# Kernel tuning notes

Measured on AMD Instinct MI355X. Metric: run time of the kernel, lower is better.

The kernel has to match this reference:

```python
import jax, jax.numpy as jnp
import numpy as np

BIT = 64
N_CLASS = 100
NUM_TRAIN = 100000
BATCH = 512
MU = 1.0   # config['mu']
M = 1.0    # config['m']
ETA = 0.5  # config['eta']
VUL = 1.0  # config['vul']
NTA = 1.0  # config['nta']


def setup_inputs() -> dict:
    key = jax.random.key(0)
    k1, k2, k3, k4, k5, k6 = jax.random.split(key, 6)
    u = jax.random.normal(k1, (BATCH, BIT), jnp.float32)
    # y / Y are one-hot label matrices in DFH; build realistic one-hot floats
    labels = jax.random.randint(k2, (BATCH,), 0, N_CLASS)
    y = jax.nn.one_hot(labels, N_CLASS, dtype=jnp.float32)
    ind = jax.random.randint(k3, (BATCH,), 0, NUM_TRAIN)
    U = jax.random.normal(k4, (BIT, NUM_TRAIN), jnp.float32)
    train_labels = jax.random.randint(k5, (NUM_TRAIN,), 0, N_CLASS)
    Y = jax.nn.one_hot(train_labels, N_CLASS, dtype=jnp.float32).T  # [n_class, num_train]
    V = jax.random.normal(k6, (BIT, N_CLASS), jnp.float32)
    return {"u": u, "y": y, "ind": ind, "U": U, "Y": Y, "V": V}


def _center_gradient(V, y, b):
    # 200-step gradient descent on V minimizing intra + vul*inter + nta*quant.
    n_class = V.shape[1]
    TK = V.shape[0] * (2.0 * jnp.eye(n_class, dtype=V.dtype)
                       - jnp.ones((n_class, n_class), V.dtype))
    yt = y.T  # [n_class, batch]

    def inner_loss(Vc):
        intra = jnp.mean((Vc @ yt - b) ** 2)
        inter = jnp.mean((Vc.T @ Vc - TK) ** 2)
        quant = jnp.mean((Vc - jnp.sign(Vc)) ** 2)
        return intra + VUL * inter + NTA * quant

    grad_fn = jax.grad(inner_loss)

    def step(Vc, i):
        # torch code multiplies alpha by 0.1 *before* the update at i==149 and i==179
        alpha = 0.03 * jnp.where(i >= 149, 0.1, 1.0) * jnp.where(i >= 179, 0.1, 1.0)
        return Vc - alpha * grad_fn(Vc), None

    V_new, _ = jax.lax.scan(step, V, jnp.arange(200))
    return V_new


def reference(u, y, ind, U, Y, V):
    # state buffer updates (torch: self.U[:, ind] = u.t().data, etc.)
    U = U.at[:, ind].set(u.T)
    Y = Y.at[:, ind].set(y.T)
    C = jnp.sign(V)
    b = jnp.sign(MU * (C @ y.T) + u.T)                     # [bit, batch]
    V_new = _center_gradient(V, y, b)                      # updated self.V
    s = (y @ Y > 0).astype(u.dtype)                        # [batch, num_train]
    ip = jnp.clip(0.5 * (u @ U), -100.0, 50.0)             # [batch, num_train]
    metric_loss = jnp.mean((1.0 - s) * jnp.log1p(jnp.exp(M + ip))
                           + s * jnp.log1p(jnp.exp(M - ip)))
    quantization_loss = jnp.mean((b - u.T) ** 2)
    loss = metric_loss + ETA * quantization_loss
    return loss, V_new
```

## Files before the change

kernel.cpp:

```cpp
#include <hip/hip_runtime.h>

#define BIT 64
#define NCLASS 100
#define NTRAIN 100000
#define BATCH 512

#define O_OWNER   0
#define O_LAB     200000
#define O_BSUM    233280
#define O_COUNT   239680
#define O_QSUM    239780
#define O_MSUM    239782

typedef __attribute__((ext_vector_type(8))) short short8v;
typedef __attribute__((ext_vector_type(4))) float f32x4;
typedef unsigned short ushortT;

__device__ __forceinline__ float signf(float x) {
    return (x > 0.f) ? 1.f : ((x < 0.f) ? -1.f : 0.f);
}

__device__ __forceinline__ unsigned cvtpk(float lo, float hi) {
    unsigned r;
    asm("v_cvt_pk_bf16_f32 %0, %1, %2" : "=v"(r) : "v"(lo), "v"(hi));
    return r;
}
__device__ __forceinline__ float dpp_x1(float x) {
    union { float f; int i; } v; v.f = x;
    v.i = __builtin_amdgcn_mov_dpp(v.i, 0xB1, 0xF, 0xF, false);
    return v.f;
}
__device__ __forceinline__ float dpp_x2(float x) {
    union { float f; int i; } v; v.f = x;
    v.i = __builtin_amdgcn_mov_dpp(v.i, 0x4E, 0xF, 0xF, false);
    return v.f;
}

__global__ __launch_bounds__(512) void k_pre(
        const float* __restrict__ y, const int* __restrict__ ind,
        const float* __restrict__ u, const float* __restrict__ V,
        int* owner, int* lab, float* Bsum, float* count, double* qsum) {
    __shared__ float srow[BATCH];
    __shared__ int   labl[BATCH];
    __shared__ double wq[8];
    const int r = blockIdx.x;
    const int bb = threadIdx.x;

    const float* yrow = y + bb * NCLASS;
    int best = 0;
    for (int c = 0; c < NCLASS; ++c)
        if (yrow[c] > 0.5f) best = c;
    labl[bb] = best;
    if (r == 0) {
        lab[bb] = best;
        atomicMax(&owner[ind[bb]], bb);
    }

    const float v  = V[r * NCLASS + best];
    const float uu = u[bb * BIT + r];
    const float bv = signf(signf(v) + uu);
    srow[bb] = bv;
    const float d = bv - uu;
    double q = (double)(d * d);
    for (int off = 32; off; off >>= 1) q += __shfl_down(q, off);
    const int wid = bb >> 6, lane = bb & 63;
    if (lane == 0) wq[wid] = q;
    __syncthreads();
    if (bb == 0) {
        double s = 0;
        for (int w = 0; w < 8; ++w) s += wq[w];
        atomicAdd(qsum, s);
    }

    if (bb < NCLASS) {
        float s = 0.f; int n = 0;
        for (int k = 0; k < BATCH; ++k) {
            const bool hit = (labl[k] == bb);
            s += hit ? srow[k] : 0.f;
            n += hit;
        }
        Bsum[r * NCLASS + bb] = s;
        if (r == 0) count[bb] = (float)n;
    }
}

__global__ __launch_bounds__(512, 2) void k_main(
        const float* __restrict__ V, const float* __restrict__ Bsum,
        const float* __restrict__ count, const float* __restrict__ u,
        const float* __restrict__ U, const float* __restrict__ Y,
        const int* __restrict__ lab, const int* __restrict__ owner,
        double* msum, float* __restrict__ out) {
    __shared__ __align__(16) char smem[81920];

    if (blockIdx.x == 0) {
        ushortT* SAb = (ushortT*)smem;
        ushortT* SBb = (ushortT*)(smem + 32768);
        ushortT* SMf = (ushortT*)(smem + 61440);
        float*   rs  = (float*)(smem + 69632);

        const int t = threadIdx.x, l = t & 63, w = t >> 6;
        const int g = l >> 4, c16 = l & 15;
        const int h = w >> 2;
        const int mtile = w & 3;
        const int m = mtile * 16 + c16;
        const bool dg = ((mtile >> 1) == h);
        const short8v ONES = {0x3F80,0x3F80,0x3F80,0x3F80,
                              0x3F80,0x3F80,0x3F80,0x3F80};

        for (int i = t; i < 16384; i += 512) SAb[i] = 0;
        for (int i = t; i < 14336; i += 512) SBb[i] = 0;

        const float ci = 2.0f / 32768.0f;
        const float ce = 4.0f / 10000.0f;
        const float cq = 2.0f / 6400.0f;
        const float ce64 = 64.0f * ce;

        bool live[4], wact[4];
        int sbO[4];
        float vreg[4][4], Kc[4][4], ncib[4][4];
        #pragma unroll
        for (int q = 0; q < 4; ++q) {
            const int nt = 4 * h + q;
            const int n0 = nt * 16 + 4 * g;
            wact[q] = (nt < 7);
            live[q] = wact[q] && (n0 < NCLASS);
            sbO[q] = ((nt * 2 + (mtile >> 1)) * 64 +
                      (16 * (c16 >> 2) + 4 * g + (c16 & 3))) * 8 + 4 * (mtile & 1);
            #pragma unroll
            for (int r = 0; r < 4; ++r) {
                float v = 0.f, bs = 0.f, cn = 0.f;
                if (live[q]) {
                    const int n = n0 + r;
                    v  = V[m * NCLASS + n];
                    bs = Bsum[m * NCLASS + n];
                    cn = count[n];
                }
                vreg[q][r] = v;
                Kc[q][r]   = ci * cn + cq - 128.f * ce;
                ncib[q][r] = -ci * bs;
            }
        }
        const int saO0 = (mtile * 4 + 2 * h) * 512 + l * 8;
        const int saO1 = saO0 + 512;

        uint4 waA, waB;

        auto store_frags = [&](ushortT* SAn, ushortT* SBn) {
            waA.x = cvtpk(vreg[0][0], vreg[0][1]);
            waA.y = cvtpk(vreg[0][2], vreg[0][3]);
            waA.z = cvtpk(vreg[1][0], vreg[1][1]);
            waA.w = cvtpk(vreg[1][2], vreg[1][3]);
            *(uint4*)&SAn[saO0] = waA;
            waB.x = cvtpk(vreg[2][0], vreg[2][1]);
            waB.y = cvtpk(vreg[2][2], vreg[2][3]);
            waB.z = cvtpk(vreg[3][0], vreg[3][1]);
            waB.w = cvtpk(vreg[3][2], vreg[3][3]);
            *(uint4*)&SAn[saO1] = waB;
            #pragma unroll
            for (int q = 0; q < 4; ++q) {
                if (wact[q]) {
                    float a0 = vreg[q][0], a1 = vreg[q][1];
                    float a2 = vreg[q][2], a3 = vreg[q][3];
                    float t0 = dpp_x1(a1), t1 = dpp_x1(a0);
                    float t2 = dpp_x1(a3), t3 = dpp_x1(a2);
                    const bool o1 = (l & 1);
                    float c0 = o1 ? t0 : a0;
                    float c1 = o1 ? a1 : t1;
                    float c2 = o1 ? t2 : a2;
                    float c3 = o1 ? a3 : t3;
                    float u0 = dpp_x2(c2), u1 = dpp_x2(c3);
                    float u2 = dpp_x2(c0), u3 = dpp_x2(c1);
                    const bool o2 = (l & 2);
                    float d0 = o2 ? u0 : c0;
                    float d1 = o2 ? u1 : c1;
                    float d2 = o2 ? c2 : u2;
                    float d3 = o2 ? c3 : u3;
                    uint2 wb;
                    wb.x = cvtpk(d0, d1);
                    wb.y = cvtpk(d2, d3);
                    *(uint2*)&SBn[sbO[q]] = wb;
                }
            }
        };

        __syncthreads();
        store_frags(SAb, SBb);
        __syncthreads();

        int cur = 0;
        for (int step = 0; step < 200; ++step) {
            float alpha = 0.03f;
            if (step >= 149) alpha *= 0.1f;
            if (step >= 179) alpha *= 0.1f;

            const ushortT* SAc = SAb + cur * 8192;
            const ushortT* SBc = SBb + cur * 7168;

            short8v a0[4], a1[4], bx0, bx1;
            #pragma unroll
            for (int ks = 0; ks < 4; ++ks) {
                a0[ks] = *(const short8v*)&SAc[(2 * h) * 2048 + ks * 512 + l * 8];
                a1[ks] = *(const short8v*)&SAc[(2 * h + 1) * 2048 + ks * 512 + l * 8];
            }
            {
                const int ko = 2 * (1 - h);
                bx0 = *(const short8v*)&SAc[mtile * 2048 + ko * 512 + l * 8];
                bx1 = *(const short8v*)&SAc[mtile * 2048 + (ko + 1) * 512 + l * 8];
            }
            short8v aP[4][2];
            #pragma unroll
            for (int q = 0; q < 4; ++q) {
                if (wact[q]) {
                    #pragma unroll
                    for (int kb = 0; kb < 2; ++kb)
                        aP[q][kb] = *(const short8v*)
                            &SBc[((4 * h + q) * 2 + kb) * 512 + l * 8];
                }
            }

            f32x4 aM0 = {0.f,0.f,0.f,0.f}, aM1 = {0.f,0.f,0.f,0.f};
            f32x4 aR  = {0.f,0.f,0.f,0.f};
            #pragma unroll
            for (int ks = 0; ks < 4; ++ks) {
                short8v b;
                if (ks == 2 * h)          b = *(const short8v*)&waA;
                else if (ks == 2 * h + 1) b = *(const short8v*)&waB;
                else if (ks == 2 * (1 - h)) b = bx0;
                else                        b = bx1;
                aM0 = __builtin_amdgcn_mfma_f32_16x16x32_bf16(a0[ks], b, aM0, 0, 0, 0);
                aM1 = __builtin_amdgcn_mfma_f32_16x16x32_bf16(a1[ks], b, aM1, 0, 0, 0);
                if (dg)
                    aR = __builtin_amdgcn_mfma_f32_16x16x32_bf16(b, ONES, aR, 0, 0, 0);
            }
            uint4 smpack;
            smpack.x = cvtpk(aM0[0], aM0[1]);
            smpack.y = cvtpk(aM0[2], aM0[3]);
            smpack.z = cvtpk(aM1[0], aM1[1]);
            smpack.w = cvtpk(aM1[2], aM1[3]);
            *(uint4*)&SMf[(mtile * 2 + h) * 512 + l * 8] = smpack;
            if (dg && c16 == 0)
                *(f32x4*)&rs[mtile * 16 + 4 * g] = aR;
            __syncthreads();

            uint4 smo = *(const uint4*)&SMf[(mtile * 2 + (1 - h)) * 512 + l * 8];
            const short8v bP0 = h ? *(const short8v*)&smo : *(const short8v*)&smpack;
            const short8v bP1 = h ? *(const short8v*)&smpack : *(const short8v*)&smo;
            f32x4 p[4];
            #pragma unroll
            for (int q = 0; q < 4; ++q) p[q] = (f32x4){0.f,0.f,0.f,0.f};
            #pragma unroll
            for (int q = 0; q < 4; ++q) {
                if (wact[q]) {
                    p[q] = __builtin_amdgcn_mfma_f32_16x16x32_bf16(aP[q][0], bP0, p[q], 0, 0, 0);
                    p[q] = __builtin_amdgcn_mfma_f32_16x16x32_bf16(aP[q][1], bP1, p[q], 0, 0, 0);
                }
            }
            const float rsm = rs[m];

            #pragma unroll
            for (int q = 0; q < 4; ++q) {
                if (wact[q]) {
                    #pragma unroll
                    for (int r = 0; r < 4; ++r) {
                        const float v = vreg[q][r];
                        float t1 = __builtin_fmaf(Kc[q][r], v, ncib[q][r]);
                        t1 = __builtin_fmaf(ce,   p[q][r], t1);
                        t1 = __builtin_fmaf(ce64, rsm,     t1);
                        t1 -= __builtin_copysignf(cq, v);
                        float vn = __builtin_fmaf(-alpha, t1, v);
                        vreg[q][r] = live[q] ? vn : 0.f;
                    }
                }
            }
            store_frags(SAb + (cur ^ 1) * 8192, SBb + (cur ^ 1) * 7168);
            __syncthreads();
            cur ^= 1;
        }

        #pragma unroll
        for (int q = 0; q < 4; ++q) {
            if (live[q]) {
                const int n0 = (4 * h + q) * 16 + 4 * g;
                #pragma unroll
                for (int r = 0; r < 4; ++r)
                    out[1 + m * NCLASS + n0 + r] = vreg[q][r];
            }
        }
    } else {
        float*  ut   = (float*)smem;
        int*    slab = (int*)(smem + 34816);
        double* wsum = (double*)(smem + 36864);
        int*    tls  = (int*)(smem + 36928);

        const int t = threadIdx.x;
        const int jj = t & 255;
        const int j = (blockIdx.x - 1) * 256 + jj;
        const int half = t >> 8;
        const bool jok = (j < NTRAIN);
        slab[t] = lab[t];

        if (half == 0) {
            int tl = 0;
            if (jok) {
                for (int c = 0; c < NCLASS; ++c)
                    if (Y[(size_t)c * NTRAIN + j] > 0.5f) tl = c;
                int ow = owner[j];
                if (ow >= 0) tl = lab[ow];
            }
            tls[jj] = tl;
        }
        __syncthreads();
        const int tl = tls[jj];

        const float* colbase = U;
        size_t cstride = NTRAIN;
        if (jok) {
            int ow = owner[j];
            if (ow >= 0) { colbase = u + (size_t)ow * BIT; cstride = 1; }
            else         { colbase = U + j; }
        }

        float lsum = 0.f;
        for (int ch = 0; ch < 4; ++ch) {
            __syncthreads();
            for (int i = t; i < 8192; i += 512) {
                int buf = i >> 12, k = (i >> 6) & 63, r = i & 63;
                ut[buf * 4352 + r * 68 + k] = u[((buf * 4 + ch) * 64 + k) * BIT + r];
            }
            __syncthreads();

            if (jok) {
                const float* myut = ut + half * 4352;
                float acc[64];
                #pragma unroll
                for (int k = 0; k < 64; ++k) acc[k] = 0.f;
                #pragma unroll 2
                for (int r = 0; r < BIT; ++r) {
                    float Uv = colbase[(size_t)r * cstride];
                    const float* urow = &myut[r * 68];
                    #pragma unroll
                    for (int qq = 0; qq < 16; ++qq) {
                        float4 uv = *(const float4*)&urow[qq * 4];
                        acc[4 * qq + 0] += uv.x * Uv;
                        acc[4 * qq + 1] += uv.y * Uv;
                        acc[4 * qq + 2] += uv.z * Uv;
                        acc[4 * qq + 3] += uv.w * Uv;
                    }
                }
                const int b0 = (half * 4 + ch) * 64;
                #pragma unroll
                for (int k = 0; k < 64; ++k) {
                    float ip = fminf(fmaxf(0.5f * acc[k], -100.f), 50.f);
                    float x = (slab[b0 + k] == tl) ? (1.0f - ip) : (1.0f + ip);
                    lsum += fmaxf(x, 0.f) + __logf(1.f + __expf(-fabsf(x)));
                }
            }
        }

        double d = (double)lsum;
        for (int off = 32; off; off >>= 1) d += __shfl_down(d, off);
        const int wid = t >> 6, lane = t & 63;
        if (lane == 0) wsum[wid] = d;
        __syncthreads();
        if (t == 0) {
            double s = 0;
            for (int ww = 0; ww < 8; ++ww) s += wsum[ww];
            atomicAdd(msum, s);
        }
    }
}

__global__ void k_final(const double* __restrict__ msum,
                        const double* __restrict__ qsum, float* out) {
    if (threadIdx.x == 0) {
        double loss = (*msum) / ((double)BATCH * (double)NTRAIN)
                    + 0.5 * ((*qsum) / ((double)BIT * (double)BATCH));
        out[0] = (float)loss;
    }
}

extern "C" void kernel_launch(void* const* d_in, const int* in_sizes, int n_in,
                              void* d_out, int out_size, void* d_ws, size_t ws_size,
                              hipStream_t stream) {
    const float* u   = (const float*)d_in[0];
    const float* y   = (const float*)d_in[1];
    const int*   ind = (const int*)d_in[2];
    const float* U   = (const float*)d_in[3];
    const float* Y   = (const float*)d_in[4];
    const float* V   = (const float*)d_in[5];
    float* out = (float*)d_out;

    int*   wsI = (int*)d_ws;
    float* wsF = (float*)d_ws;
    int*   owner = wsI + O_OWNER;
    int*   lab   = wsI + O_LAB;
    float* Bsum  = wsF + O_BSUM;
    float* count = wsF + O_COUNT;
    double* qsum = (double*)(wsF + O_QSUM);
    double* msum = (double*)(wsF + O_MSUM);

    hipMemsetAsync(owner, 0xFF, NTRAIN * sizeof(int), stream);
    hipMemsetAsync(wsF + O_QSUM, 0, 4 * sizeof(float), stream);

    k_pre<<<64, 512, 0, stream>>>(y, ind, u, V, owner, lab, Bsum, count, qsum);
    k_main<<<1 + (NTRAIN + 255) / 256, 512, 0, stream>>>(
        V, Bsum, count, u, U, Y, lab, owner, msum, out);
    k_final<<<1, 64, 0, stream>>>(msum, qsum, out);
}
```

Measured before the change: 394.3 us.

## Compute full Gram tile redundantly per wave to drop per-step LDS exchange and barrier

In the 200-step center-gradient loop, each wave now computes all four 16-row tiles of its Gram column redundantly instead of half. It also always computes the row-sum MFMA. This removes the shared-memory staging buffer used to swap Gram halves between wave pairs and the __syncthreads that guarded it, shortening the serial per-step critical path. The cost is roughly twice the Gram MFMAs and more LDS fragment reads per wave, plus a smaller shared-memory footprint.

```diff
diff --git a/kernel.cpp b/kernel.cpp
--- a/kernel.cpp
+++ b/kernel.cpp
@@ -90,20 +90,18 @@
         const float* __restrict__ U, const float* __restrict__ Y,
         const int* __restrict__ lab, const int* __restrict__ owner,
         double* msum, float* __restrict__ out) {
-    __shared__ __align__(16) char smem[81920];
+    __shared__ __align__(16) char smem[70144];
 
     if (blockIdx.x == 0) {
         ushortT* SAb = (ushortT*)smem;
         ushortT* SBb = (ushortT*)(smem + 32768);
-        ushortT* SMf = (ushortT*)(smem + 61440);
-        float*   rs  = (float*)(smem + 69632);
+        float*   rs  = (float*)(smem + 61440);
 
         const int t = threadIdx.x, l = t & 63, w = t >> 6;
         const int g = l >> 4, c16 = l & 15;
         const int h = w >> 2;
         const int mtile = w & 3;
         const int m = mtile * 16 + c16;
-        const bool dg = ((mtile >> 1) == h);
         const short8v ONES = {0x3F80,0x3F80,0x3F80,0x3F80,
                               0x3F80,0x3F80,0x3F80,0x3F80};
 
@@ -196,63 +194,57 @@
             const ushortT* SAc = SAb + cur * 8192;
             const ushortT* SBc = SBb + cur * 7168;
 
-            short8v a0[4], a1[4], bx0, bx1;
+            short8v bfr[4];
             #pragma unroll
             for (int ks = 0; ks < 4; ++ks) {
-                a0[ks] = *(const short8v*)&SAc[(2 * h) * 2048 + ks * 512 + l * 8];
-                a1[ks] = *(const short8v*)&SAc[(2 * h + 1) * 2048 + ks * 512 + l * 8];
-            }
-            {
-                const int ko = 2 * (1 - h);
-                bx0 = *(const short8v*)&SAc[mtile * 2048 + ko * 512 + l * 8];
-                bx1 = *(const short8v*)&SAc[mtile * 2048 + (ko + 1) * 512 + l * 8];
-            }
-            short8v aP[4][2];
+                if (ks == 2 * h)          bfr[ks] = *(const short8v*)&waA;
+                else if (ks == 2 * h + 1) bfr[ks] = *(const short8v*)&waB;
+                else bfr[ks] = *(const short8v*)&SAc[mtile * 2048 + ks * 512 + l * 8];
+            }
+
+            f32x4 accm[4];
+            #pragma unroll
+            for (int rp = 0; rp < 4; ++rp) {
+                accm[rp] = (f32x4){0.f,0.f,0.f,0.f};
+                #pragma unroll
+                for (int ks = 0; ks < 4; ++ks) {
+                    short8v afr = (rp == mtile) ? bfr[ks]
+                        : *(const short8v*)&SAc[rp * 2048 + ks * 512 + l * 8];
+                    accm[rp] = __builtin_amdgcn_mfma_f32_16x16x32_bf16(
+                        afr, bfr[ks], accm[rp], 0, 0, 0);
+                }
+            }
+            f32x4 aR = {0.f,0.f,0.f,0.f};
+            #pragma unroll
+            for (int ks = 0; ks < 4; ++ks)
+                aR = __builtin_amdgcn_mfma_f32_16x16x32_bf16(bfr[ks], ONES, aR, 0, 0, 0);
+            if (c16 == 0)
+                *(f32x4*)&rs[mtile * 16 + 4 * g] = aR;
+
+            uint4 bPw0, bPw1;
+            bPw0.x = cvtpk(accm[0][0], accm[0][1]);
+            bPw0.y = cvtpk(accm[0][2], accm[0][3]);
+            bPw0.z = cvtpk(accm[1][0], accm[1][1]);
+            bPw0.w = cvtpk(accm[1][2], accm[1][3]);
+            bPw1.x = cvtpk(accm[2][0], accm[2][1]);
+            bPw1.y = cvtpk(accm[2][2], accm[2][3]);
+            bPw1.z = cvtpk(accm[3][0], accm[3][1]);
+            bPw1.w = cvtpk(accm[3][2], accm[3][3]);
+            const short8v bP0 = *(const short8v*)&bPw0;
+            const short8v bP1 = *(const short8v*)&bPw1;
+
+            f32x4 p[4];
+            #pragma unroll
+            for (int q = 0; q < 4; ++q) p[q] = (f32x4){0.f,0.f,0.f,0.f};
             #pragma unroll
             for (int q = 0; q < 4; ++q) {
                 if (wact[q]) {
-                    #pragma unroll
-                    for (int kb = 0; kb < 2; ++kb)
-                        aP[q][kb] = *(const short8v*)
-                            &SBc[((4 * h + q) * 2 + kb) * 512 + l * 8];
-                }
-            }
-
-            f32x4 aM0 = {0.f,0.f,0.f,0.f}, aM1 = {0.f,0.f,0.f,0.f};
-            f32x4 aR  = {0.f,0.f,0.f,0.f};
-            #pragma unroll
-            for (int ks = 0; ks < 4; ++ks) {
-                short8v b;
-                if (ks == 2 * h)          b = *(const short8v*)&waA;
-                else if (ks == 2 * h + 1) b = *(const short8v*)&waB;
-                else if (ks == 2 * (1 - h)) b = bx0;
-                else                        b = bx1;
-                aM0 = __builtin_amdgcn_mfma_f32_16x16x32_bf16(a0[ks], b, aM0, 0, 0, 0);
-                aM1 = __builtin_amdgcn_mfma_f32_16x16x32_bf16(a1[ks], b, aM1, 0, 0, 0);
-                if (dg)
-                    aR = __builtin_amdgcn_mfma_f32_16x16x32_bf16(b, ONES, aR, 0, 0, 0);
-            }
-            uint4 smpack;
-            smpack.x = cvtpk(aM0[0], aM0[1]);
-            smpack.y = cvtpk(aM0[2], aM0[3]);
-            smpack.z = cvtpk(aM1[0], aM1[1]);
-            smpack.w = cvtpk(aM1[2], aM1[3]);
-            *(uint4*)&SMf[(mtile * 2 + h) * 512 + l * 8] = smpack;
-            if (dg && c16 == 0)
-                *(f32x4*)&rs[mtile * 16 + 4 * g] = aR;
-            __syncthreads();
-
-            uint4 smo = *(const uint4*)&SMf[(mtile * 2 + (1 - h)) * 512 + l * 8];
-            const short8v bP0 = h ? *(const short8v*)&smo : *(const short8v*)&smpack;
-            const short8v bP1 = h ? *(const short8v*)&smpack : *(const short8v*)&smo;
-            f32x4 p[4];
-            #pragma unroll
-            for (int q = 0; q < 4; ++q) p[q] = (f32x4){0.f,0.f,0.f,0.f};
-            #pragma unroll
-            for (int q = 0; q < 4; ++q) {
-                if (wact[q]) {
-                    p[q] = __builtin_amdgcn_mfma_f32_16x16x32_bf16(aP[q][0], bP0, p[q], 0, 0, 0);
-                    p[q] = __builtin_amdgcn_mfma_f32_16x16x32_bf16(aP[q][1], bP1, p[q], 0, 0, 0);
+                    short8v aP0 = *(const short8v*)
+                        &SBc[((4 * h + q) * 2 + 0) * 512 + l * 8];
+                    short8v aP1 = *(const short8v*)
+                        &SBc[((4 * h + q) * 2 + 1) * 512 + l * 8];
+                    p[q] = __builtin_amdgcn_mfma_f32_16x16x32_bf16(aP0, bP0, p[q], 0, 0, 0);
+                    p[q] = __builtin_amdgcn_mfma_f32_16x16x32_bf16(aP1, bP1, p[q], 0, 0, 0);
                 }
             }
             const float rsm = rs[m];
```

New measurement: 409.1 us. +3.8%, slower.

## Read pre-transposed u from global instead of staging in LDS; shrink center-GD register footprint

Applied to the files above, without the earlier changes.

k_pre now writes a transposed copy of u into workspace. The metric blocks read it directly with wave-uniform addresses, which drops the per-chunk LDS staging, its two barriers, and the shared label copy. Shared memory per block shrinks, which may let more blocks fit per CU. The center-gradient block now loads MFMA operands inside the loops rather than preloading them into registers, trading register pressure for extra LDS reads. The risk is that global/scalar-cache reads of uT and lab may be slower than LDS reads.

```diff
diff --git a/kernel.cpp b/kernel.cpp
--- a/kernel.cpp
+++ b/kernel.cpp
@@ -7,6 +7,7 @@
 
 #define O_OWNER   0
 #define O_LAB     200000
+#define O_UT      200512
 #define O_BSUM    233280
 #define O_COUNT   239680
 #define O_QSUM    239780
@@ -39,7 +40,8 @@
 __global__ __launch_bounds__(512) void k_pre(
         const float* __restrict__ y, const int* __restrict__ ind,
         const float* __restrict__ u, const float* __restrict__ V,
-        int* owner, int* lab, float* Bsum, float* count, double* qsum) {
+        int* owner, int* lab, float* Bsum, float* count, double* qsum,
+        float* uT) {
     __shared__ float srow[BATCH];
     __shared__ int   labl[BATCH];
     __shared__ double wq[8];
@@ -58,6 +60,7 @@
 
     const float v  = V[r * NCLASS + best];
     const float uu = u[bb * BIT + r];
+    uT[r * BATCH + bb] = uu;
     const float bv = signf(signf(v) + uu);
     srow[bb] = bv;
     const float d = bv - uu;
@@ -89,8 +92,8 @@
         const float* __restrict__ count, const float* __restrict__ u,
         const float* __restrict__ U, const float* __restrict__ Y,
         const int* __restrict__ lab, const int* __restrict__ owner,
-        double* msum, float* __restrict__ out) {
-    __shared__ __align__(16) char smem[81920];
+        const float* __restrict__ uT, double* msum, float* __restrict__ out) {
+    __shared__ __align__(16) char smem[70144];
 
     if (blockIdx.x == 0) {
         ushortT* SAb = (ushortT*)smem;
@@ -194,65 +197,45 @@
             if (step >= 179) alpha *= 0.1f;
 
             const ushortT* SAc = SAb + cur * 8192;
-            const ushortT* SBc = SBb + cur * 7168;
-
-            short8v a0[4], a1[4], bx0, bx1;
-            #pragma unroll
-            for (int ks = 0; ks < 4; ++ks) {
-                a0[ks] = *(const short8v*)&SAc[(2 * h) * 2048 + ks * 512 + l * 8];
-                a1[ks] = *(const short8v*)&SAc[(2 * h + 1) * 2048 + ks * 512 + l * 8];
-            }
-            {
-                const int ko = 2 * (1 - h);
-                bx0 = *(const short8v*)&SAc[mtile * 2048 + ko * 512 + l * 8];
-                bx1 = *(const short8v*)&SAc[mtile * 2048 + (ko + 1) * 512 + l * 8];
-            }
-            short8v aP[4][2];
-            #pragma unroll
-            for (int q = 0; q < 4; ++q) {
-                if (wact[q]) {
-                    #pragma unroll
-                    for (int kb = 0; kb < 2; ++kb)
-                        aP[q][kb] = *(const short8v*)
-                            &SBc[((4 * h + q) * 2 + kb) * 512 + l * 8];
-                }
-            }
 
             f32x4 aM0 = {0.f,0.f,0.f,0.f}, aM1 = {0.f,0.f,0.f,0.f};
             f32x4 aR  = {0.f,0.f,0.f,0.f};
             #pragma unroll
             for (int ks = 0; ks < 4; ++ks) {
-                short8v b;
-                if (ks == 2 * h)          b = *(const short8v*)&waA;
-                else if (ks == 2 * h + 1) b = *(const short8v*)&waB;
-                else if (ks == 2 * (1 - h)) b = bx0;
-                else                        b = bx1;
-                aM0 = __builtin_amdgcn_mfma_f32_16x16x32_bf16(a0[ks], b, aM0, 0, 0, 0);
-                aM1 = __builtin_amdgcn_mfma_f32_16x16x32_bf16(a1[ks], b, aM1, 0, 0, 0);
+                short8v b  = *(const short8v*)&SAc[mtile * 2048 + ks * 512 + l * 8];
+                short8v a0 = *(const short8v*)&SAc[(2 * h) * 2048 + ks * 512 + l * 8];
+                short8v a1 = *(const short8v*)&SAc[(2 * h + 1) * 2048 + ks * 512 + l * 8];
+                aM0 = __builtin_amdgcn_mfma_f32_16x16x32_bf16(a0, b, aM0, 0, 0, 0);
+                aM1 = __builtin_amdgcn_mfma_f32_16x16x32_bf16(a1, b, aM1, 0, 0, 0);
                 if (dg)
                     aR = __builtin_amdgcn_mfma_f32_16x16x32_bf16(b, ONES, aR, 0, 0, 0);
             }
-            uint4 smpack;
-            smpack.x = cvtpk(aM0[0], aM0[1]);
-            smpack.y = cvtpk(aM0[2], aM0[3]);
-            smpack.z = cvtpk(aM1[0], aM1[1]);
-            smpack.w = cvtpk(aM1[2], aM1[3]);
-            *(uint4*)&SMf[(mtile * 2 + h) * 512 + l * 8] = smpack;
+            {
+                uint4 sm;
+                sm.x = cvtpk(aM0[0], aM0[1]);
+                sm.y = cvtpk(aM0[2], aM0[3]);
+                sm.z = cvtpk(aM1[0], aM1[1]);
+                sm.w = cvtpk(aM1[2], aM1[3]);
+                *(uint4*)&SMf[(mtile * 2 + h) * 512 + l * 8] = sm;
+            }
             if (dg && c16 == 0)
                 *(f32x4*)&rs[mtile * 16 + 4 * g] = aR;
             __syncthreads();
 
-            uint4 smo = *(const uint4*)&SMf[(mtile * 2 + (1 - h)) * 512 + l * 8];
-            const short8v bP0 = h ? *(const short8v*)&smo : *(const short8v*)&smpack;
-            const short8v bP1 = h ? *(const short8v*)&smpack : *(const short8v*)&smo;
+            const ushortT* SBc = SBb + cur * 7168;
             f32x4 p[4];
             #pragma unroll
             for (int q = 0; q < 4; ++q) p[q] = (f32x4){0.f,0.f,0.f,0.f};
             #pragma unroll
-            for (int q = 0; q < 4; ++q) {
-                if (wact[q]) {
-                    p[q] = __builtin_amdgcn_mfma_f32_16x16x32_bf16(aP[q][0], bP0, p[q], 0, 0, 0);
-                    p[q] = __builtin_amdgcn_mfma_f32_16x16x32_bf16(aP[q][1], bP1, p[q], 0, 0, 0);
+            for (int kb = 0; kb < 2; ++kb) {
+                short8v bP = *(const short8v*)&SMf[(mtile * 2 + kb) * 512 + l * 8];
+                #pragma unroll
+                for (int q = 0; q < 4; ++q) {
+                    if (wact[q]) {
+                        short8v aP = *(const short8v*)
+                            &SBc[((4 * h + q) * 2 + kb) * 512 + l * 8];
+                        p[q] = __builtin_amdgcn_mfma_f32_16x16x32_bf16(aP, bP, p[q], 0, 0, 0);
+                    }
                 }
             }
             const float rsm = rs[m];
@@ -287,17 +270,14 @@
             }
         }
     } else {
-        float*  ut   = (float*)smem;
-        int*    slab = (int*)(smem + 34816);
-        double* wsum = (double*)(smem + 36864);
-        int*    tls  = (int*)(smem + 36928);
+        double* wsum = (double*)(smem);
+        int*    tls  = (int*)(smem + 64);
 
         const int t = threadIdx.x;
         const int jj = t & 255;
         const int j = (blockIdx.x - 1) * 256 + jj;
         const int half = t >> 8;
         const bool jok = (j < NTRAIN);
-        slab[t] = lab[t];
 
         if (half == 0) {
             int tl = 0;
@@ -322,22 +302,16 @@
 
         float lsum = 0.f;
         for (int ch = 0; ch < 4; ++ch) {
-            __syncthreads();
-            for (int i = t; i < 8192; i += 512) {
-                int buf = i >> 12, k = (i >> 6) & 63, r = i & 63;
-                ut[buf * 4352 + r * 68 + k] = u[((buf * 4 + ch) * 64 + k) * BIT + r];
-            }
-            __syncthreads();
+            const int b0u = __builtin_amdgcn_readfirstlane((half * 4 + ch) * 64);
 
             if (jok) {
-                const float* myut = ut + half * 4352;
                 float acc[64];
                 #pragma unroll
                 for (int k = 0; k < 64; ++k) acc[k] = 0.f;
-                #pragma unroll 2
+                #pragma unroll 4
                 for (int r = 0; r < BIT; ++r) {
                     float Uv = colbase[(size_t)r * cstride];
-                    const float* urow = &myut[r * 68];
+                    const float* urow = &uT[r * BATCH + b0u];
                     #pragma unroll
                     for (int qq = 0; qq < 16; ++qq) {
                         float4 uv = *(const float4*)&urow[qq * 4];
@@ -347,11 +321,11 @@
                         acc[4 * qq + 3] += uv.w * Uv;
                     }
                 }
-                const int b0 = (half * 4 + ch) * 64;
                 #pragma unroll
                 for (int k = 0; k < 64; ++k) {
+                    const int lv = lab[b0u + k];
                     float ip = fminf(fmaxf(0.5f * acc[k], -100.f), 50.f);
-                    float x = (slab[b0 + k] == tl) ? (1.0f - ip) : (1.0f + ip);
+                    float x = (lv == tl) ? (1.0f - ip) : (1.0f + ip);
                     lsum += fmaxf(x, 0.f) + __logf(1.f + __expf(-fabsf(x)));
                 }
             }
@@ -394,6 +368,7 @@
     float* wsF = (float*)d_ws;
     int*   owner = wsI + O_OWNER;
     int*   lab   = wsI + O_LAB;
+    float* uT    = wsF + O_UT;
     float* Bsum  = wsF + O_BSUM;
     float* count = wsF + O_COUNT;
     double* qsum = (double*)(wsF + O_QSUM);
@@ -402,8 +377,8 @@
     hipMemsetAsync(owner, 0xFF, NTRAIN * sizeof(int), stream);
     hipMemsetAsync(wsF + O_QSUM, 0, 4 * sizeof(float), stream);
 
-    k_pre<<<64, 512, 0, stream>>>(y, ind, u, V, owner, lab, Bsum, count, qsum);
+    k_pre<<<64, 512, 0, stream>>>(y, ind, u, V, owner, lab, Bsum, count, qsum, uT);
     k_main<<<1 + (NTRAIN + 255) / 256, 512, 0, stream>>>(
-        V, Bsum, count, u, U, Y, lab, owner, msum, out);
+        V, Bsum, count, u, U, Y, lab, owner, uT, msum, out);
     k_final<<<1, 64, 0, stream>>>(msum, qsum, out);
 }
```

Measured after the change: 436.3 us. 10.7% more time.
